# Performance work log

Measured on AMD Instinct MI355X. Metric: run time of the kernel, lower is better.

## Reference

```python
import jax, jax.numpy as jnp
import numpy as np

WS = (2, 7, 7)   # window size (d, h, w)
SS = (1, 3, 3)   # shift size
EPS = 1e-5


def _rel_pos_index(ws):
    d, h, w = np.arange(ws[0]), np.arange(ws[1]), np.arange(ws[2])
    coords = np.stack(np.meshgrid(d, h, w, indexing='ij'))        # (3, wd, wh, ww)
    flat = coords.reshape(3, -1)                                   # (3, N)
    rel = flat[:, :, None] - flat[:, None, :]                      # (3, N, N)
    rel = rel.transpose(1, 2, 0).astype(np.int64)                  # (N, N, 3)
    rel[:, :, 0] += ws[0] - 1
    rel[:, :, 1] += ws[1] - 1
    rel[:, :, 2] += ws[2] - 1
    rel[:, :, 0] *= (2 * ws[1] - 1) * (2 * ws[2] - 1)
    rel[:, :, 1] *= 2 * ws[2] - 1
    return rel.sum(-1)                                             # (N, N)


def _window_partition(x, ws):
    B, D, H, W, C = x.shape
    x = x.reshape(B, D // ws[0], ws[0], H // ws[1], ws[1], W // ws[2], ws[2], C)
    return x.transpose(0, 1, 3, 5, 2, 4, 6, 7).reshape(-1, ws[0] * ws[1] * ws[2], C)


def _window_reverse(win, ws, B, D, H, W):
    x = win.reshape(B, D // ws[0], H // ws[1], W // ws[2], ws[0], ws[1], ws[2], -1)
    return x.transpose(0, 1, 4, 2, 5, 3, 6, 7).reshape(B, D, H, W, -1)


def _attn_mask(D, H, W, ws, ss):
    img = np.zeros((1, D, H, W, 1), np.float32)
    cnt = 0
    for dsl in (slice(None, -ws[0]), slice(-ws[0], -ss[0]), slice(-ss[0], None)):
        for hsl in (slice(None, -ws[1]), slice(-ws[1], -ss[1]), slice(-ss[1], None)):
            for wsl in (slice(None, -ws[2]), slice(-ws[2], -ss[2]), slice(-ss[2], None)):
                img[:, dsl, hsl, wsl, :] = cnt
                cnt += 1
    mw = _window_partition(img, ws)[..., 0]                        # (nW, N)
    am = mw[:, None, :] - mw[:, :, None]                           # (nW, N, N)
    return np.where(am != 0, np.float32(-100.0), np.float32(0.0))


def _ln(x, g, b):
    m = x.mean(-1, keepdims=True)
    v = ((x - m) ** 2).mean(-1, keepdims=True)
    return (x - m) / jnp.sqrt(v + EPS) * g + b


def setup_inputs():
    key = jax.random.key(0)
    B, D, H, W, C = 2, 8, 56, 56, 256
    nH, hidden = 8, 1024
    ks = jax.random.split(key, 8)
    s = 0.02
    inp = {
        'x': jax.random.normal(ks[0], (B, D, H, W, C), jnp.float32),
        'qkv_w': jax.random.normal(ks[1], (3 * C, C), jnp.float32) * s,
        'qkv_b': jnp.zeros((3 * C,), jnp.float32),
        'proj_w': jax.random.normal(ks[2], (C, C), jnp.float32) * s,
        'proj_b': jnp.zeros((C,), jnp.float32),
        'rpb_table': jax.random.normal(ks[3], (3 * 13 * 13, nH), jnp.float32) * s,
        'ln1_g': jnp.ones((C,), jnp.float32),
        'ln1_b': jnp.zeros((C,), jnp.float32),
        'ln2_g': jnp.ones((C,), jnp.float32),
        'ln2_b': jnp.zeros((C,), jnp.float32),
        'fc1_w': jax.random.normal(ks[4], (hidden, C), jnp.float32) * s,
        'fc1_b': jnp.zeros((hidden,), jnp.float32),
        'fc2_w': jax.random.normal(ks[5], (C, hidden), jnp.float32) * s,
        'fc2_b': jnp.zeros((C,), jnp.float32),
        'rel_idx': jnp.asarray(_rel_pos_index(WS), jnp.int32),
        'attn_mask': jnp.asarray(_attn_mask(D, H, W, WS, SS)),
        'num_heads': nH,
    }
    return inp


def reference(x, qkv_w, qkv_b, proj_w, proj_b, rpb_table, ln1_g, ln1_b, ln2_g,
              ln2_b, fc1_w, fc1_b, fc2_w, fc2_b, rel_idx, attn_mask, num_heads):
    B, D, H, W, C = x.shape
    N = WS[0] * WS[1] * WS[2]
    hd = C // num_heads
    scale = hd ** (-0.5)

    shortcut = x
    h = _ln(x, ln1_g, ln1_b)
    # cyclic shift
    h = jnp.roll(h, shift=(-SS[0], -SS[1], -SS[2]), axis=(1, 2, 3))
    win = _window_partition(h, WS)                                 # (B_, N, C)

    qkv = win @ qkv_w.T + qkv_b                                    # (B_, N, 3C)
    qkv = qkv.reshape(-1, N, 3, num_heads, hd).transpose(2, 0, 3, 1, 4)
    q, k, v = qkv[0] * scale, qkv[1], qkv[2]                       # (B_, nH, N, hd)

    attn = jnp.einsum('bhid,bhjd->bhij', q, k)                     # (B_, nH, N, N)
    bias = rpb_table[rel_idx.reshape(-1)].reshape(N, N, num_heads).transpose(2, 0, 1)
    attn = attn + bias[None]
    nW = attn_mask.shape[0]
    attn = attn.reshape(B, nW, num_heads, N, N) + attn_mask[None, :, None]
    attn = jax.nn.softmax(attn.reshape(-1, num_heads, N, N), axis=-1)

    out = jnp.einsum('bhij,bhjd->bhid', attn, v)                   # (B_, nH, N, hd)
    out = out.transpose(0, 2, 1, 3).reshape(-1, N, C)
    out = out @ proj_w.T + proj_b

    xr = _window_reverse(out, WS, B, D, H, W)
    xr = jnp.roll(xr, shift=SS, axis=(1, 2, 3))                    # reverse shift
    x = shortcut + xr

    h2 = _ln(x, ln2_g, ln2_b)
    m = jax.nn.gelu(h2 @ fc1_w.T + fc1_b, approximate=False)
    m = m @ fc2_w.T + fc2_b
    return x + m
```

## Files before the change

kernel.cpp:

```cpp
#include <hip/hip_runtime.h>
#include <hip/hip_bf16.h>
#include <math.h>

#define B_  2
#define D_  8
#define H_  56
#define W_  56
#define C_  256
#define NH_ 8
#define HD_ 32
#define N_  98
#define NWIN_TOT 512
#define TOK (B_*D_*H_*W_)
#define HID 1024

typedef short bf16x8 __attribute__((ext_vector_type(8)));
typedef float f32x4  __attribute__((ext_vector_type(4)));

__device__ __forceinline__ ushort f2b(float f) {
    union { __hip_bfloat16 h; ushort u; } v;
    v.h = __float2bfloat16(f);
    return v.u;
}
__device__ __forceinline__ float b2f(ushort h) {
    union { unsigned u; float f; } v; v.u = ((unsigned)h) << 16;
    return v.f;
}

__device__ __forceinline__ void glds16(const void* gsrc, void* lds_dst) {
    __builtin_amdgcn_global_load_lds(
        (const __attribute__((address_space(1))) unsigned int*)gsrc,
        (__attribute__((address_space(3))) unsigned int*)lds_dst,
        16, 0, 0);
}

__device__ __forceinline__ int tok_of_winrow(int r) {
    int wid  = r / N_;
    int n    = r - wid * N_;
    int b    = wid >> 8;
    int rem  = wid & 255;
    int di   = rem >> 6;
    int hi   = (rem >> 3) & 7;
    int wi   = rem & 7;
    int wd   = n / 49;
    int rem2 = n - wd * 49;
    int wh   = rem2 / 7;
    int ww   = rem2 - wh * 7;
    int d = di * 2 + wd + 1; if (d >= D_) d -= D_;
    int h = hi * 7 + wh + 3; if (h >= H_) h -= H_;
    int w = wi * 7 + ww + 3; if (w >= W_) w -= W_;
    return ((b * D_ + d) * H_ + h) * W_ + w;
}

__device__ __forceinline__ float gelu_fast(float x) {
    float y = 1.5957691216057308f * (x + 0.044715f * x * x * x);
    return x / (1.0f + __expf(-y));
}

template<bool GATHER>
__global__ __launch_bounds__(256)
void ln_kernel(const float* __restrict__ x, const float* __restrict__ g,
               const float* __restrict__ bta, ushort* __restrict__ out, int nrows) {
    int wave = blockIdx.x * 4 + (threadIdx.x >> 6);
    int lane = threadIdx.x & 63;
    if (wave >= nrows) return;
    int srow = GATHER ? tok_of_winrow(wave) : wave;
    float4 v = ((const float4*)(x + (size_t)srow * C_))[lane];
    float s  = v.x + v.y + v.z + v.w;
    float ss = v.x*v.x + v.y*v.y + v.z*v.z + v.w*v.w;
    #pragma unroll
    for (int o = 32; o; o >>= 1) { s += __shfl_xor(s, o); ss += __shfl_xor(ss, o); }
    float mean = s * (1.0f / C_);
    float var  = ss * (1.0f / C_) - mean * mean;
    float rstd = rsqrtf(var + 1e-5f);
    float4 gg = ((const float4*)g)[lane];
    float4 bb = ((const float4*)bta)[lane];
    ushort4 o4;
    o4.x = f2b((v.x - mean) * rstd * gg.x + bb.x);
    o4.y = f2b((v.y - mean) * rstd * gg.y + bb.y);
    o4.z = f2b((v.z - mean) * rstd * gg.z + bb.z);
    o4.w = f2b((v.w - mean) * rstd * gg.w + bb.w);
    ((ushort4*)(out + (size_t)wave * C_))[lane] = o4;
}

#define TB2_WORDS (8 * 8 * 7 * 14 * 64)
__global__ void tbl_kernel(const int* __restrict__ rel_idx,
                           const float* __restrict__ rpb,
                           const float* __restrict__ mask,
                           uint* __restrict__ Tb2) {
    int idx = blockIdx.x * blockDim.x + threadIdx.x;
    if (idx >= TB2_WORDS) return;
    int lane = idx & 63;
    int t    = idx >> 6;
    int nq   = t % 14;  int t2 = t / 14;
    int mi   = t2 % 7;  int ph = t2 / 7;
    int pat  = ph >> 3, hh = ph & 7;
    int nj   = nq >> 1, q = nq & 1;
    int lrow = lane & 15, lgrp = lane >> 4;
    int j  = nj * 16 + lrow;
    int i0 = mi * 16 + lgrp * 4 + q * 2;
    int di = (pat & 1) ? 3 : 0, hi = (pat & 2) ? 7 : 0, wi = (pat & 4) ? 7 : 0;
    int rep = di * 64 + hi * 8 + wi;
    float lo = -1e30f, hv = -1e30f;
    if (j < N_) {
        if (i0 < N_)
            lo = rpb[rel_idx[i0 * N_ + j] * NH_ + hh] + mask[(size_t)rep * (N_*N_) + i0 * N_ + j];
        if (i0 + 1 < N_)
            hv = rpb[rel_idx[(i0+1) * N_ + j] * NH_ + hh] + mask[(size_t)rep * (N_*N_) + (i0+1) * N_ + j];
    }
    Tb2[idx] = (uint)f2b(lo) | ((uint)f2b(hv) << 16);
}

__global__ void f2b4_kernel(const float* __restrict__ s0, ushort* __restrict__ d0, int n0,
                            const float* __restrict__ s1, ushort* __restrict__ d1, int n1,
                            const float* __restrict__ s2, ushort* __restrict__ d2, int n2,
                            const float* __restrict__ s3, ushort* __restrict__ d3, int n3) {
    const float* s; ushort* d; int n;
    switch (blockIdx.y) {
        case 0: s = s0; d = d0; n = n0; break;
        case 1: s = s1; d = d1; n = n1; break;
        case 2: s = s2; d = d2; n = n2; break;
        default: s = s3; d = d3; n = n3; break;
    }
    int i = (blockIdx.x * blockDim.x + threadIdx.x) * 4;
    if (i >= n) return;
    float4 v = *(const float4*)(s + i);
    ushort4 o; o.x = f2b(v.x); o.y = f2b(v.y); o.z = f2b(v.z); o.w = f2b(v.w);
    *(ushort4*)(d + i) = o;
}

template<int MODE>
__global__ __launch_bounds__(256)
void gemm_bf16(const ushort* __restrict__ A, const ushort* __restrict__ Wm,
               const float* __restrict__ bias, void* __restrict__ Cout,
               const void* __restrict__ resid, int M, int K, int Nout) {
    __shared__ __align__(16) char lds[32768];
    char* ldsA = lds;
    char* ldsB = lds + 16384;
    const int tid  = threadIdx.x;
    const int wv   = tid >> 6, lane = tid & 63;
    const int m0   = blockIdx.x * 128, n0 = blockIdx.y * 128;
    const int wrow = (wv >> 1) * 64, wcol = (wv & 1) * 64;
    const int lr8  = lane >> 3, lc = lane & 7;

    f32x4 acc[4][4] = {};

    const ushort* Ag[4]; const ushort* Bg[4];
    #pragma unroll
    for (int i = 0; i < 4; ++i) {
        int row = (wv * 4 + i) * 8 + lr8;
        int gc  = lc ^ (row & 7);
        Ag[i] = A  + (size_t)(m0 + row) * K + gc * 8;
        Bg[i] = Wm + (size_t)(n0 + row) * K + gc * 8;
    }

    for (int k0 = 0; k0 < K; k0 += 64) {
        #pragma unroll
        for (int i = 0; i < 4; ++i) {
            glds16(Ag[i] + k0, ldsA + (wv * 4 + i) * 1024);
            glds16(Bg[i] + k0, ldsB + (wv * 4 + i) * 1024);
        }
        __syncthreads();
        #pragma unroll
        for (int kk = 0; kk < 2; ++kk) {
            bf16x8 af[4], bfr[4];
            #pragma unroll
            for (int i = 0; i < 4; ++i) {
                int r = wrow + i * 16 + (lane & 15);
                int c = (lane >> 4) + kk * 4;
                af[i]  = *(const bf16x8*)(ldsA + r * 128 + ((c ^ (r & 7)) * 16));
                int r2 = wcol + i * 16 + (lane & 15);
                bfr[i] = *(const bf16x8*)(ldsB + r2 * 128 + ((c ^ (r2 & 7)) * 16));
            }
            #pragma unroll
            for (int i = 0; i < 4; ++i)
                #pragma unroll
                for (int j = 0; j < 4; ++j)
                    acc[i][j] = __builtin_amdgcn_mfma_f32_16x16x32_bf16(af[i], bfr[j], acc[i][j], 0, 0, 0);
        }
        __syncthreads();
    }

    int colg[4]; float bv[4];
    #pragma unroll
    for (int j = 0; j < 4; ++j) {
        colg[j] = n0 + wcol + j * 16 + (lane & 15);
        bv[j]   = bias[colg[j]];
    }
    #pragma unroll
    for (int i = 0; i < 4; ++i) {
        #pragma unroll
        for (int r = 0; r < 4; ++r) {
            int rowg = m0 + wrow + i * 16 + ((lane >> 4) << 2) + r;
            #pragma unroll
            for (int j = 0; j < 4; ++j) {
                float v = acc[i][j][r] + bv[j];
                if (MODE == 0) {
                    ((ushort*)Cout)[(size_t)rowg * Nout + colg[j]] = f2b(v);
                } else if (MODE == 2) {
                    ((ushort*)Cout)[(size_t)rowg * Nout + colg[j]] = f2b(gelu_fast(v));
                } else {
                    v += ((const float*)resid)[(size_t)rowg * Nout + colg[j]];
                    ((float*)Cout)[(size_t)rowg * Nout + colg[j]] = v;
                }
            }
        }
    }
}

__global__ __launch_bounds__(256)
void gemm_proj_ln(const ushort* __restrict__ A, const ushort* __restrict__ Wm,
                  const float* __restrict__ pbias, const float* __restrict__ x,
                  const float* __restrict__ g2, const float* __restrict__ b2,
                  float* __restrict__ out, ushort* __restrict__ h2) {
    __shared__ __align__(16) char lds[49152];
    __shared__ float stats[4][64][2];
    char* ldsA = lds;
    char* ldsB = lds + 16384;
    const int tid  = threadIdx.x;
    const int wv   = tid >> 6, lane = tid & 63;
    const int lrow = lane & 15, lgrp = lane >> 4;
    const int m0   = blockIdx.x * 128;
    const int wrow = (wv >> 1) * 64, wcol = (wv & 1) * 128;
    const int lr8  = lane >> 3, lc = lane & 7;

    f32x4 acc[4][8] = {};

    for (int k0 = 0; k0 < 256; k0 += 64) {
        #pragma unroll
        for (int i = 0; i < 4; ++i) {
            int row = (wv * 4 + i) * 8 + lr8;
            int gc  = lc ^ (row & 7);
            glds16(A + (size_t)(m0 + row) * 256 + k0 + gc * 8, ldsA + (wv * 4 + i) * 1024);
        }
        #pragma unroll
        for (int i = 0; i < 8; ++i) {
            int row = (wv * 8 + i) * 8 + lr8;
            int gc  = lc ^ (row & 7);
            glds16(Wm + (size_t)row * 256 + k0 + gc * 8, ldsB + (wv * 8 + i) * 1024);
        }
        __syncthreads();
        #pragma unroll
        for (int kk = 0; kk < 2; ++kk) {
            bf16x8 af[4], bfr[8];
            #pragma unroll
            for (int i = 0; i < 4; ++i) {
                int r = wrow + i * 16 + lrow;
                af[i] = *(const bf16x8*)(ldsA + r * 128 + (((lgrp + kk * 4) ^ (r & 7)) * 16));
            }
            #pragma unroll
            for (int j = 0; j < 8; ++j) {
                int r2 = wcol + j * 16 + lrow;
                bfr[j] = *(const bf16x8*)(ldsB + r2 * 128 + (((lgrp + kk * 4) ^ (r2 & 7)) * 16));
            }
            #pragma unroll
            for (int i = 0; i < 4; ++i)
                #pragma unroll
                for (int j = 0; j < 8; ++j)
                    acc[i][j] = __builtin_amdgcn_mfma_f32_16x16x32_bf16(af[i], bfr[j], acc[i][j], 0, 0, 0);
        }
        __syncthreads();
    }

    int colg[8]; float bvj[8];
    #pragma unroll
    for (int j = 0; j < 8; ++j) {
        colg[j] = wcol + j * 16 + lrow;
        bvj[j]  = pbias[colg[j]];
    }
    int tokr[4][4];

    #pragma unroll
    for (int i = 0; i < 4; ++i) {
        #pragma unroll
        for (int r = 0; r < 4; ++r) {
            int rowg = m0 + wrow + i * 16 + lgrp * 4 + r;
            int tok  = tok_of_winrow(rowg);
            tokr[i][r] = tok;
            float s = 0.f, sq = 0.f;
            #pragma unroll
            for (int j = 0; j < 8; ++j) {
                float v = acc[i][j][r] + bvj[j] + x[(size_t)tok * C_ + colg[j]];
                acc[i][j][r] = v;
                out[(size_t)tok * C_ + colg[j]] = v;
                s += v; sq += v * v;
            }
            #pragma unroll
            for (int o = 1; o < 16; o <<= 1) { s += __shfl_xor(s, o); sq += __shfl_xor(sq, o); }
            if (lrow == 0) {
                int lrw = i * 16 + lgrp * 4 + r;
                stats[wv][lrw][0] = s;
                stats[wv][lrw][1] = sq;
            }
        }
    }
    __syncthreads();

    float gj[8], bj[8];
    #pragma unroll
    for (int j = 0; j < 8; ++j) { gj[j] = g2[colg[j]]; bj[j] = b2[colg[j]]; }
    #pragma unroll
    for (int i = 0; i < 4; ++i) {
        #pragma unroll
        for (int r = 0; r < 4; ++r) {
            int lrw = i * 16 + lgrp * 4 + r;
            float s  = stats[wv][lrw][0] + stats[wv ^ 1][lrw][0];
            float sq = stats[wv][lrw][1] + stats[wv ^ 1][lrw][1];
            float mean = s * (1.0f / 256.0f);
            float var  = sq * (1.0f / 256.0f) - mean * mean;
            float rstd = rsqrtf(var + 1e-5f);
            int tok = tokr[i][r];
            #pragma unroll
            for (int j = 0; j < 8; ++j) {
                float v = (acc[i][j][r] - mean) * rstd * gj[j] + bj[j];
                h2[(size_t)tok * C_ + colg[j]] = f2b(v);
            }
        }
    }
}

#define KOFF 0
#define VOFF 7168
#define POFF 15360
#define SMEM_BYTES 32768
__global__ __launch_bounds__(256)
void attn_mfma(const ushort* __restrict__ qkv, const uint* __restrict__ Tb2,
               ushort* __restrict__ attn_out) {
    __shared__ __align__(16) char smem[SMEM_BYTES];
    ushort (*Pl)[16][136] = (ushort (*)[16][136])(smem + POFF);
    const int b    = blockIdx.x;
    const int wid  = (b & 7) + ((b >> 6) << 3);
    const int hh   = (b >> 3) & 7;
    const int tid  = threadIdx.x;
    const int wv   = tid >> 6, lane = tid & 63;
    const int lrow = lane & 15, lgrp = lane >> 4;
    const float scale = 0.17677669529663687f;

    const ushort* base = qkv + (size_t)wid * N_ * 768 + hh * 32;
    const int rem = wid & 255;
    const int pat = (((rem >> 6) == 3) ? 1 : 0) | ((((rem >> 3) & 7) == 7) ? 2 : 0)
                  | (((rem & 7) == 7) ? 4 : 0);
    const uint* tb2 = Tb2 + (size_t)((pat * 8 + hh) * 7) * 14 * 64 + lane;

    {
        uint4 z = {0, 0, 0, 0};
        uint4* l4 = (uint4*)(smem + 14336);
        for (int i = tid; i < (SMEM_BYTES - 14336) / 16; i += 256) l4[i] = z;
    }
    __syncthreads();

    #pragma unroll
    for (int sect = 0; sect < 2; ++sect) {
        char* dstbase = smem + sect * 7168;
        const ushort* src = base + 256 + sect * 256;
        for (int c = tid; c < 448; c += 256) {
            int r = c >> 2; if (r > 97) r = 97;
            int cc = c & 3;
            glds16(src + (size_t)r * 768 + ((cc ^ (r & 3)) * 8), dstbase + c * 16);
        }
    }
    __syncthreads();

    const int swz = (lgrp ^ (lrow & 3)) << 4;

    bf16x8 kf[7];
    #pragma unroll
    for (int nj = 0; nj < 7; ++nj)
        kf[nj] = *(const bf16x8*)(smem + KOFF + (nj * 16 + lrow) * 64 + swz);

    bf16x8 vf[2][4];
    #pragma unroll
    for (int dt = 0; dt < 2; ++dt)
        #pragma unroll
        for (int kt = 0; kt < 4; ++kt) {
            bf16x8 tmp;
            #pragma unroll
            for (int t = 0; t < 8; ++t) {
                int R = kt * 32 + lgrp * 8 + t;
                int q = dt * 2 + (lrow >> 3);
                tmp[t] = *(const short*)(smem + VOFF + R * 64 +
                                         ((q ^ (t & 3)) << 4) + ((lrow & 7) << 1));
            }
            vf[dt][kt] = tmp;
        }

    for (int mi = wv; mi < 7; mi += 4) {
        const int ibase = mi * 16;

        uint tw[14];
        const uint* tbm = tb2 + mi * 14 * 64;
        #pragma unroll
        for (int u = 0; u < 14; ++u) tw[u] = tbm[u * 64];

        bf16x8 qf = *(const bf16x8*)(base + (size_t)(ibase + lrow) * 768 + lgrp * 8);

        f32x4 s[7];
        #pragma unroll
        for (int nj = 0; nj < 7; ++nj) {
            f32x4 z = {0.f, 0.f, 0.f, 0.f};
            s[nj] = __builtin_amdgcn_mfma_f32_16x16x32_bf16(qf, kf[nj], z, 0, 0, 0);
        }

        #pragma unroll
        for (int nj = 0; nj < 7; ++nj) {
            #pragma unroll
            for (int r = 0; r < 4; ++r) {
                uint w = tw[nj * 2 + (r >> 1)];
                ushort hb = (r & 1) ? (ushort)(w >> 16) : (ushort)(w & 0xffff);
                s[nj][r] = s[nj][r] * scale + b2f(hb);
            }
        }

        float rinv[4];
        #pragma unroll
        for (int r = 0; r < 4; ++r) {
            float acc = 0.f;
            #pragma unroll
            for (int nj = 0; nj < 7; ++nj) {
                float p = __expf(s[nj][r]);
                s[nj][r] = p;
                acc += p;
            }
            #pragma unroll
            for (int o = 1; o < 16; o <<= 1) acc += __shfl_xor(acc, o);
            rinv[r] = 1.f / acc;
        }

        #pragma unroll
        for (int nj = 0; nj < 7; ++nj)
            #pragma unroll
            for (int r = 0; r < 4; ++r)
                Pl[wv][lgrp * 4 + r][nj * 16 + lrow] = f2b(s[nj][r] * rinv[r]);

        f32x4 o0 = {0.f, 0.f, 0.f, 0.f}, o1 = {0.f, 0.f, 0.f, 0.f};
        #pragma unroll
        for (int kt = 0; kt < 4; ++kt) {
            bf16x8 pf = *(const bf16x8*)(&Pl[wv][lrow][kt * 32 + lgrp * 8]);
            o0 = __builtin_amdgcn_mfma_f32_16x16x32_bf16(pf, vf[0][kt], o0, 0, 0, 0);
            o1 = __builtin_amdgcn_mfma_f32_16x16x32_bf16(pf, vf[1][kt], o1, 0, 0, 0);
        }

        #pragma unroll
        for (int r = 0; r < 4; ++r) {
            int i = ibase + lgrp * 4 + r;
            if (i < N_) {
                size_t rb = ((size_t)(wid * N_ + i)) * C_ + hh * 32;
                attn_out[rb + lrow]      = f2b(o0[r]);
                attn_out[rb + 16 + lrow] = f2b(o1[r]);
            }
        }
    }
}

extern "C" void kernel_launch(void* const* d_in, const int* in_sizes, int n_in,
                              void* d_out, int out_size, void* d_ws, size_t ws_size,
                              hipStream_t stream) {
    const float* x      = (const float*)d_in[0];
    const float* qkv_w  = (const float*)d_in[1];
    const float* qkv_b  = (const float*)d_in[2];
    const float* proj_w = (const float*)d_in[3];
    const float* proj_b = (const float*)d_in[4];
    const float* rpb    = (const float*)d_in[5];
    const float* ln1_g  = (const float*)d_in[6];
    const float* ln1_b  = (const float*)d_in[7];
    const float* ln2_g  = (const float*)d_in[8];
    const float* ln2_b  = (const float*)d_in[9];
    const float* fc1_w  = (const float*)d_in[10];
    const float* fc1_b  = (const float*)d_in[11];
    const float* fc2_w  = (const float*)d_in[12];
    const float* fc2_b  = (const float*)d_in[13];
    const int*   rel_idx= (const int*)d_in[14];
    const float* mask   = (const float*)d_in[15];
    float* out = (float*)d_out;

    char* ws = (char*)d_ws;
    ushort* regionA = (ushort*)ws;
    ushort* regionB = (ushort*)(ws + (size_t)TOK * HID * 2);
    ushort* wq  = (ushort*)(ws + (size_t)TOK * HID * 2 + (size_t)TOK * C_ * 2);
    ushort* wp  = wq + 768 * 256;
    ushort* w1  = wp + 256 * 256;
    ushort* w2  = w1 + HID * 256;
    uint*   Tb2 = (uint*)(w2 + 256 * HID);
    ushort* h2buf = (ushort*)((char*)Tb2 + TB2_WORDS * 4);

    tbl_kernel<<<(TB2_WORDS + 255) / 256, 256, 0, stream>>>(rel_idx, rpb, mask, Tb2);
    {
        dim3 g(256, 4);
        f2b4_kernel<<<g, 256, 0, stream>>>(qkv_w, wq, 768 * 256,
                                           proj_w, wp, 256 * 256,
                                           fc1_w, w1, HID * 256,
                                           fc2_w, w2, 256 * HID);
    }

    ln_kernel<true><<<TOK / 4, 256, 0, stream>>>(x, ln1_g, ln1_b, regionB, TOK);

    {
        dim3 g(TOK / 128, 768 / 128);
        gemm_bf16<0><<<g, 256, 0, stream>>>(regionB, wq, qkv_b, regionA, nullptr, TOK, 256, 768);
    }

    attn_mfma<<<NWIN_TOT * NH_, 256, 0, stream>>>(regionA, Tb2, regionB);

    gemm_proj_ln<<<TOK / 128, 256, 0, stream>>>(regionB, wp, proj_b, x,
                                                ln2_g, ln2_b, out, h2buf);

    {
        dim3 g(TOK / 128, HID / 128);
        gemm_bf16<2><<<g, 256, 0, stream>>>(h2buf, w1, fc1_b, regionA, nullptr, TOK, 256, HID);
    }

    {
        dim3 g(TOK / 128, 256 / 128);
        gemm_bf16<3><<<g, 256, 0, stream>>>(regionA, w2, fc2_b, out, out, TOK, HID, 256);
    }
}
```

Baseline: 266.2 us.

## Fuse MLP fc1+GELU+fc2 into one kernel and stage QKV stores through LDS

Replaces the two MLP GEMM launches with one fused kernel. Each 64-token block keeps its LN2 output in LDS, computes fc1 in 128-wide hidden chunks, applies GELU into LDS, and accumulates fc2 in registers, so the 1024-wide hidden activation never goes to global memory. The fused kernel reads w1 and w2 fragments straight from global memory, without LDS staging or double buffering, which may make it latency-bound. Separately, the QKV GEMM epilogue now writes results through a swizzled LDS tile so that global stores are 16-byte coalesced.

New measurement: 342.8 us. +28.8%, slower.

```diff
diff --git a/kernel.cpp b/kernel.cpp
--- a/kernel.cpp
+++ b/kernel.cpp
@@ -129,11 +129,10 @@
     *(ushort4*)(d + i) = o;
 }
 
-template<int MODE>
 __global__ __launch_bounds__(256)
-void gemm_bf16(const ushort* __restrict__ A, const ushort* __restrict__ Wm,
-               const float* __restrict__ bias, void* __restrict__ Cout,
-               const void* __restrict__ resid, int M, int K, int Nout) {
+void gemm_qkv(const ushort* __restrict__ A, const ushort* __restrict__ Wm,
+              const float* __restrict__ bias, ushort* __restrict__ Cout,
+              int K, int Nout) {
     __shared__ __align__(16) char lds[32768];
     char* ldsA = lds;
     char* ldsB = lds + 16384;
@@ -142,6 +141,7 @@
     const int m0   = blockIdx.x * 128, n0 = blockIdx.y * 128;
     const int wrow = (wv >> 1) * 64, wcol = (wv & 1) * 64;
     const int lr8  = lane >> 3, lc = lane & 7;
+    const int lrow = lane & 15, lgrp = lane >> 4;
 
     f32x4 acc[4][4] = {};
 
@@ -166,10 +166,10 @@
             bf16x8 af[4], bfr[4];
             #pragma unroll
             for (int i = 0; i < 4; ++i) {
-                int r = wrow + i * 16 + (lane & 15);
-                int c = (lane >> 4) + kk * 4;
+                int r = wrow + i * 16 + lrow;
+                int c = lgrp + kk * 4;
                 af[i]  = *(const bf16x8*)(ldsA + r * 128 + ((c ^ (r & 7)) * 16));
-                int r2 = wcol + i * 16 + (lane & 15);
+                int r2 = wcol + i * 16 + lrow;
                 bfr[i] = *(const bf16x8*)(ldsB + r2 * 128 + ((c ^ (r2 & 7)) * 16));
             }
             #pragma unroll
@@ -181,30 +181,32 @@
         __syncthreads();
     }
 
-    int colg[4]; float bv[4];
-    #pragma unroll
-    for (int j = 0; j < 4; ++j) {
-        colg[j] = n0 + wcol + j * 16 + (lane & 15);
-        bv[j]   = bias[colg[j]];
-    }
+    float bv[4];
+    #pragma unroll
+    for (int j = 0; j < 4; ++j) bv[j] = bias[n0 + wcol + j * 16 + lrow];
+
     #pragma unroll
     for (int i = 0; i < 4; ++i) {
         #pragma unroll
         for (int r = 0; r < 4; ++r) {
-            int rowg = m0 + wrow + i * 16 + ((lane >> 4) << 2) + r;
+            int row_l = wrow + i * 16 + lgrp * 4 + r;
             #pragma unroll
             for (int j = 0; j < 4; ++j) {
-                float v = acc[i][j][r] + bv[j];
-                if (MODE == 0) {
-                    ((ushort*)Cout)[(size_t)rowg * Nout + colg[j]] = f2b(v);
-                } else if (MODE == 2) {
-                    ((ushort*)Cout)[(size_t)rowg * Nout + colg[j]] = f2b(gelu_fast(v));
-                } else {
-                    v += ((const float*)resid)[(size_t)rowg * Nout + colg[j]];
-                    ((float*)Cout)[(size_t)rowg * Nout + colg[j]] = v;
-                }
-            }
-        }
+                int col_l = wcol + j * 16 + lrow;
+                int cchunk = (col_l >> 3) ^ (row_l & 7);
+                *(ushort*)(lds + row_l * 256 + (cchunk << 4) + ((col_l & 7) << 1)) =
+                    f2b(acc[i][j][r] + bv[j]);
+            }
+        }
+    }
+    __syncthreads();
+
+    #pragma unroll
+    for (int it = 0; it < 8; ++it) {
+        int li  = tid + it * 256;
+        int row = li >> 4, c = li & 15;
+        uint4 v = *(const uint4*)(lds + row * 256 + ((c ^ (row & 7)) << 4));
+        *(uint4*)(Cout + (size_t)(m0 + row) * Nout + n0 + c * 8) = v;
     }
 }
 
@@ -314,6 +316,114 @@
             for (int j = 0; j < 8; ++j) {
                 float v = (acc[i][j][r] - mean) * rstd * gj[j] + bj[j];
                 h2[(size_t)tok * C_ + colg[j]] = f2b(v);
+            }
+        }
+    }
+}
+
+__global__ __launch_bounds__(256)
+void gemm_mlp(const ushort* __restrict__ h2, const ushort* __restrict__ w1,
+              const float* __restrict__ b1, const ushort* __restrict__ w2,
+              const float* __restrict__ b2, float* __restrict__ out) {
+    __shared__ __align__(16) char ldsA[32768];
+    __shared__ __align__(16) char ldsH[16384];
+    const int tid  = threadIdx.x;
+    const int wv   = tid >> 6, lane = tid & 63;
+    const int lrow = lane & 15, lgrp = lane >> 4;
+    const int m0   = blockIdx.x * 64;
+    const int wr   = wv >> 1, wc = wv & 1;
+
+    #pragma unroll
+    for (int it = 0; it < 8; ++it) {
+        int ci  = tid + it * 256;
+        int row = ci >> 5, d = ci & 31;
+        glds16(h2 + (size_t)(m0 + row) * 256 + ((d ^ (row & 7)) * 8), ldsA + ci * 16);
+    }
+    __syncthreads();
+
+    f32x4 acc2[4][4] = {};
+
+    for (int hc = 0; hc < 8; ++hc) {
+        f32x4 acc1[2][4] = {};
+        #pragma unroll
+        for (int ks = 0; ks < 8; ++ks) {
+            bf16x8 af[2], bfr[4];
+            #pragma unroll
+            for (int i = 0; i < 2; ++i) {
+                int row = wr * 32 + i * 16 + lrow;
+                int c   = ks * 4 + lgrp;
+                af[i] = *(const bf16x8*)(ldsA + row * 512 + ((c ^ (row & 7)) << 4));
+            }
+            #pragma unroll
+            for (int j = 0; j < 4; ++j) {
+                int hr = hc * 128 + wc * 64 + j * 16 + lrow;
+                bfr[j] = *(const bf16x8*)(w1 + (size_t)hr * 256 + ks * 32 + lgrp * 8);
+            }
+            #pragma unroll
+            for (int i = 0; i < 2; ++i)
+                #pragma unroll
+                for (int j = 0; j < 4; ++j)
+                    acc1[i][j] = __builtin_amdgcn_mfma_f32_16x16x32_bf16(af[i], bfr[j], acc1[i][j], 0, 0, 0);
+        }
+
+        float b1v[4];
+        #pragma unroll
+        for (int j = 0; j < 4; ++j) b1v[j] = b1[hc * 128 + wc * 64 + j * 16 + lrow];
+
+        __syncthreads();
+        #pragma unroll
+        for (int i = 0; i < 2; ++i) {
+            #pragma unroll
+            for (int j = 0; j < 4; ++j) {
+                int hid_l = wc * 64 + j * 16 + lrow;
+                #pragma unroll
+                for (int r = 0; r < 4; ++r) {
+                    int hrow = wr * 32 + i * 16 + lgrp * 4 + r;
+                    float v = gelu_fast(acc1[i][j][r] + b1v[j]);
+                    int cchunk = (hid_l >> 3) ^ (hrow & 7);
+                    *(ushort*)(ldsH + hrow * 256 + (cchunk << 4) + ((hid_l & 7) << 1)) = f2b(v);
+                }
+            }
+        }
+        __syncthreads();
+
+        #pragma unroll
+        for (int ks = 0; ks < 4; ++ks) {
+            bf16x8 af2[4], bf2[4];
+            #pragma unroll
+            for (int i = 0; i < 4; ++i) {
+                int row = i * 16 + lrow;
+                int c   = ks * 4 + lgrp;
+                af2[i] = *(const bf16x8*)(ldsH + row * 256 + ((c ^ (row & 7)) << 4));
+            }
+            #pragma unroll
+            for (int j = 0; j < 4; ++j) {
+                int cr = wv * 64 + j * 16 + lrow;
+                bf2[j] = *(const bf16x8*)(w2 + (size_t)cr * 1024 + hc * 128 + ks * 32 + lgrp * 8);
+            }
+            #pragma unroll
+            for (int i = 0; i < 4; ++i)
+                #pragma unroll
+                for (int j = 0; j < 4; ++j)
+                    acc2[i][j] = __builtin_amdgcn_mfma_f32_16x16x32_bf16(af2[i], bf2[j], acc2[i][j], 0, 0, 0);
+        }
+    }
+
+    float b2v[4]; int cg[4];
+    #pragma unroll
+    for (int j = 0; j < 4; ++j) {
+        cg[j]  = wv * 64 + j * 16 + lrow;
+        b2v[j] = b2[cg[j]];
+    }
+    #pragma unroll
+    for (int i = 0; i < 4; ++i) {
+        #pragma unroll
+        for (int r = 0; r < 4; ++r) {
+            int row = m0 + i * 16 + lgrp * 4 + r;
+            #pragma unroll
+            for (int j = 0; j < 4; ++j) {
+                float v = acc2[i][j][r] + b2v[j] + out[(size_t)row * C_ + cg[j]];
+                out[(size_t)row * C_ + cg[j]] = v;
             }
         }
     }
@@ -496,7 +606,7 @@
 
     {
         dim3 g(TOK / 128, 768 / 128);
-        gemm_bf16<0><<<g, 256, 0, stream>>>(regionB, wq, qkv_b, regionA, nullptr, TOK, 256, 768);
+        gemm_qkv<<<g, 256, 0, stream>>>(regionB, wq, qkv_b, regionA, 256, 768);
     }
 
     attn_mfma<<<NWIN_TOT * NH_, 256, 0, stream>>>(regionA, Tb2, regionB);
@@ -504,13 +614,5 @@
     gemm_proj_ln<<<TOK / 128, 256, 0, stream>>>(regionB, wp, proj_b, x,
                                                 ln2_g, ln2_b, out, h2buf);
 
-    {
-        dim3 g(TOK / 128, HID / 128);
-        gemm_bf16<2><<<g, 256, 0, stream>>>(h2buf, w1, fc1_b, regionA, nullptr, TOK, 256, HID);
-    }
-
-    {
-        dim3 g(TOK / 128, 256 / 128);
-        gemm_bf16<3><<<g, 256, 0, stream>>>(regionA, w2, fc2_b, out, out, TOK, HID, 256);
-    }
-}
+    gemm_mlp<<<TOK / 64, 256, 0, stream>>>(h2buf, w1, fc1_b, w2, fc2_b, out);
+}
```

## Double-buffer GEMM LDS tiles, linearize grid for M-tile locality, inline bf16 rounding

Applied to the files above, without the earlier changes.

The generic bf16 GEMM now double-buffers its A/B tiles in 64KB of LDS, issuing global-to-LDS loads for the next k-step before computing on the current one. This drops one barrier per iteration and overlaps load latency with MFMA work. The grid is flattened to 1D with the N-tile index varying fastest, so blocks sharing an A row-tile run close together and reuse it in cache. The float-to-bf16 conversion is replaced by a manual round-to-nearest-even bit trick, which skips NaN handling. Doubling LDS per block may lower occupancy.

After: 263.8 us. No clear change (-0.9%).

```diff
diff --git a/kernel.cpp b/kernel.cpp
--- a/kernel.cpp
+++ b/kernel.cpp
@@ -18,9 +18,9 @@
 typedef float f32x4  __attribute__((ext_vector_type(4)));
 
 __device__ __forceinline__ ushort f2b(float f) {
-    union { __hip_bfloat16 h; ushort u; } v;
-    v.h = __float2bfloat16(f);
-    return v.u;
+    union { float f; unsigned u; } v; v.f = f;
+    unsigned r = v.u + 0x7fff + ((v.u >> 16) & 1);
+    return (ushort)(r >> 16);
 }
 __device__ __forceinline__ float b2f(ushort h) {
     union { unsigned u; float f; } v; v.u = ((unsigned)h) << 16;
@@ -134,42 +134,58 @@
 void gemm_bf16(const ushort* __restrict__ A, const ushort* __restrict__ Wm,
                const float* __restrict__ bias, void* __restrict__ Cout,
                const void* __restrict__ resid, int M, int K, int Nout) {
-    __shared__ __align__(16) char lds[32768];
-    char* ldsA = lds;
-    char* ldsB = lds + 16384;
+    __shared__ __align__(16) char lds[65536];
     const int tid  = threadIdx.x;
     const int wv   = tid >> 6, lane = tid & 63;
-    const int m0   = blockIdx.x * 128, n0 = blockIdx.y * 128;
+    const int nby  = Nout >> 7;
+    const int bx   = blockIdx.x / nby, by = blockIdx.x - bx * nby;
+    const int m0   = bx * 128, n0 = by * 128;
     const int wrow = (wv >> 1) * 64, wcol = (wv & 1) * 64;
     const int lr8  = lane >> 3, lc = lane & 7;
+    const int lrow = lane & 15, lgrp = lane >> 4;
 
     f32x4 acc[4][4] = {};
 
     const ushort* Ag[4]; const ushort* Bg[4];
+    int ldoff[4];
     #pragma unroll
     for (int i = 0; i < 4; ++i) {
         int row = (wv * 4 + i) * 8 + lr8;
         int gc  = lc ^ (row & 7);
         Ag[i] = A  + (size_t)(m0 + row) * K + gc * 8;
         Bg[i] = Wm + (size_t)(n0 + row) * K + gc * 8;
-    }
-
-    for (int k0 = 0; k0 < K; k0 += 64) {
-        #pragma unroll
-        for (int i = 0; i < 4; ++i) {
-            glds16(Ag[i] + k0, ldsA + (wv * 4 + i) * 1024);
-            glds16(Bg[i] + k0, ldsB + (wv * 4 + i) * 1024);
-        }
-        __syncthreads();
+        ldoff[i] = (wv * 4 + i) * 1024;
+    }
+
+    const int nk = K >> 6;
+    #pragma unroll
+    for (int i = 0; i < 4; ++i) {
+        glds16(Ag[i], lds + ldoff[i]);
+        glds16(Bg[i], lds + 16384 + ldoff[i]);
+    }
+    __syncthreads();
+
+    int cur = 0;
+    for (int t = 0; t < nk; ++t) {
+        if (t + 1 < nk) {
+            char* nb = lds + (cur ^ 1) * 32768;
+            #pragma unroll
+            for (int i = 0; i < 4; ++i) {
+                glds16(Ag[i] + (t + 1) * 64, nb + ldoff[i]);
+                glds16(Bg[i] + (t + 1) * 64, nb + 16384 + ldoff[i]);
+            }
+        }
+        char* ldsA = lds + cur * 32768;
+        char* ldsB = ldsA + 16384;
         #pragma unroll
         for (int kk = 0; kk < 2; ++kk) {
             bf16x8 af[4], bfr[4];
             #pragma unroll
             for (int i = 0; i < 4; ++i) {
-                int r = wrow + i * 16 + (lane & 15);
-                int c = (lane >> 4) + kk * 4;
+                int r = wrow + i * 16 + lrow;
+                int c = lgrp + kk * 4;
                 af[i]  = *(const bf16x8*)(ldsA + r * 128 + ((c ^ (r & 7)) * 16));
-                int r2 = wcol + i * 16 + (lane & 15);
+                int r2 = wcol + i * 16 + lrow;
                 bfr[i] = *(const bf16x8*)(ldsB + r2 * 128 + ((c ^ (r2 & 7)) * 16));
             }
             #pragma unroll
@@ -179,19 +195,20 @@
                     acc[i][j] = __builtin_amdgcn_mfma_f32_16x16x32_bf16(af[i], bfr[j], acc[i][j], 0, 0, 0);
         }
         __syncthreads();
+        cur ^= 1;
     }
 
     int colg[4]; float bv[4];
     #pragma unroll
     for (int j = 0; j < 4; ++j) {
-        colg[j] = n0 + wcol + j * 16 + (lane & 15);
+        colg[j] = n0 + wcol + j * 16 + lrow;
         bv[j]   = bias[colg[j]];
     }
     #pragma unroll
     for (int i = 0; i < 4; ++i) {
         #pragma unroll
         for (int r = 0; r < 4; ++r) {
-            int rowg = m0 + wrow + i * 16 + ((lane >> 4) << 2) + r;
+            int rowg = m0 + wrow + i * 16 + (lgrp << 2) + r;
             #pragma unroll
             for (int j = 0; j < 4; ++j) {
                 float v = acc[i][j][r] + bv[j];
@@ -494,23 +511,17 @@
 
     ln_kernel<true><<<TOK / 4, 256, 0, stream>>>(x, ln1_g, ln1_b, regionB, TOK);
 
-    {
-        dim3 g(TOK / 128, 768 / 128);
-        gemm_bf16<0><<<g, 256, 0, stream>>>(regionB, wq, qkv_b, regionA, nullptr, TOK, 256, 768);
-    }
+    gemm_bf16<0><<<(TOK / 128) * 6, 256, 0, stream>>>(regionB, wq, qkv_b, regionA,
+                                                      nullptr, TOK, 256, 768);
 
     attn_mfma<<<NWIN_TOT * NH_, 256, 0, stream>>>(regionA, Tb2, regionB);
 
     gemm_proj_ln<<<TOK / 128, 256, 0, stream>>>(regionB, wp, proj_b, x,
                                                 ln2_g, ln2_b, out, h2buf);
 
-    {
-        dim3 g(TOK / 128, HID / 128);
-        gemm_bf16<2><<<g, 256, 0, stream>>>(h2buf, w1, fc1_b, regionA, nullptr, TOK, 256, HID);
-    }
-
-    {
-        dim3 g(TOK / 128, 256 / 128);
-        gemm_bf16<3><<<g, 256, 0, stream>>>(regionA, w2, fc2_b, out, out, TOK, HID, 256);
-    }
-}
+    gemm_bf16<2><<<(TOK / 128) * 8, 256, 0, stream>>>(h2buf, w1, fc1_b, regionA,
+                                                      nullptr, TOK, 256, HID);
+
+    gemm_bf16<3><<<(TOK / 128) * 2, 256, 0, stream>>>(regionA, w2, fc2_b, out,
+                                                      out, TOK, HID, 256);
+}
```

## Transpose MFMA output to vectorize GEMM epilogues and swap grid order

Applied to the files above, without the earlier changes.

Swaps the MFMA operand order so each lane holds four consecutive output columns of one row. This lets the GEMM and proj+LN epilogues use float4 and packed-bf16 stores and loads instead of scattered scalar accesses. It also adds a hardware packed bf16 conversion instruction and reorders the grid so blocks sharing an A row-tile run together, which should improve cache reuse of activations. It changes the LN reduction layout, which adds risk of correctness errors in the stats exchange.

Result: slower. 291.5 us (+9.5%).

```diff
diff --git a/kernel.cpp b/kernel.cpp
--- a/kernel.cpp
+++ b/kernel.cpp
@@ -18,13 +18,18 @@
 typedef float f32x4  __attribute__((ext_vector_type(4)));
 
 __device__ __forceinline__ ushort f2b(float f) {
-    union { __hip_bfloat16 h; ushort u; } v;
-    v.h = __float2bfloat16(f);
-    return v.u;
+    union { float f; unsigned u; } v; v.f = f;
+    unsigned r = v.u + 0x7fff + ((v.u >> 16) & 1);
+    return (ushort)(r >> 16);
 }
 __device__ __forceinline__ float b2f(ushort h) {
     union { unsigned u; float f; } v; v.u = ((unsigned)h) << 16;
     return v.f;
+}
+__device__ __forceinline__ uint pk2(float a, float b) {
+    uint r;
+    asm("v_cvt_pk_bf16_f32 %0, %1, %2" : "=v"(r) : "v"(a), "v"(b));
+    return r;
 }
 
 __device__ __forceinline__ void glds16(const void* gsrc, void* lds_dst) {
@@ -75,12 +80,10 @@
     float rstd = rsqrtf(var + 1e-5f);
     float4 gg = ((const float4*)g)[lane];
     float4 bb = ((const float4*)bta)[lane];
-    ushort4 o4;
-    o4.x = f2b((v.x - mean) * rstd * gg.x + bb.x);
-    o4.y = f2b((v.y - mean) * rstd * gg.y + bb.y);
-    o4.z = f2b((v.z - mean) * rstd * gg.z + bb.z);
-    o4.w = f2b((v.w - mean) * rstd * gg.w + bb.w);
-    ((ushort4*)(out + (size_t)wave * C_))[lane] = o4;
+    uint2 o2;
+    o2.x = pk2((v.x - mean) * rstd * gg.x + bb.x, (v.y - mean) * rstd * gg.y + bb.y);
+    o2.y = pk2((v.z - mean) * rstd * gg.z + bb.z, (v.w - mean) * rstd * gg.w + bb.w);
+    ((uint2*)(out + (size_t)wave * C_))[lane] = o2;
 }
 
 #define TB2_WORDS (8 * 8 * 7 * 14 * 64)
@@ -125,8 +128,8 @@
     int i = (blockIdx.x * blockDim.x + threadIdx.x) * 4;
     if (i >= n) return;
     float4 v = *(const float4*)(s + i);
-    ushort4 o; o.x = f2b(v.x); o.y = f2b(v.y); o.z = f2b(v.z); o.w = f2b(v.w);
-    *(ushort4*)(d + i) = o;
+    uint2 o; o.x = pk2(v.x, v.y); o.y = pk2(v.z, v.w);
+    *(uint2*)(d + i) = o;
 }
 
 template<int MODE>
@@ -139,9 +142,10 @@
     char* ldsB = lds + 16384;
     const int tid  = threadIdx.x;
     const int wv   = tid >> 6, lane = tid & 63;
-    const int m0   = blockIdx.x * 128, n0 = blockIdx.y * 128;
+    const int n0   = blockIdx.x * 128, m0 = blockIdx.y * 128;
     const int wrow = (wv >> 1) * 64, wcol = (wv & 1) * 64;
     const int lr8  = lane >> 3, lc = lane & 7;
+    const int lrow = lane & 15, lgrp = lane >> 4;
 
     f32x4 acc[4][4] = {};
 
@@ -166,43 +170,47 @@
             bf16x8 af[4], bfr[4];
             #pragma unroll
             for (int i = 0; i < 4; ++i) {
-                int r = wrow + i * 16 + (lane & 15);
-                int c = (lane >> 4) + kk * 4;
+                int r = wrow + i * 16 + lrow;
+                int c = lgrp + kk * 4;
                 af[i]  = *(const bf16x8*)(ldsA + r * 128 + ((c ^ (r & 7)) * 16));
-                int r2 = wcol + i * 16 + (lane & 15);
+                int r2 = wcol + i * 16 + lrow;
                 bfr[i] = *(const bf16x8*)(ldsB + r2 * 128 + ((c ^ (r2 & 7)) * 16));
             }
             #pragma unroll
             for (int i = 0; i < 4; ++i)
                 #pragma unroll
                 for (int j = 0; j < 4; ++j)
-                    acc[i][j] = __builtin_amdgcn_mfma_f32_16x16x32_bf16(af[i], bfr[j], acc[i][j], 0, 0, 0);
+                    acc[i][j] = __builtin_amdgcn_mfma_f32_16x16x32_bf16(bfr[j], af[i], acc[i][j], 0, 0, 0);
         }
         __syncthreads();
     }
 
-    int colg[4]; float bv[4];
-    #pragma unroll
-    for (int j = 0; j < 4; ++j) {
-        colg[j] = n0 + wcol + j * 16 + (lane & 15);
-        bv[j]   = bias[colg[j]];
-    }
+    float4 bv4[4];
+    #pragma unroll
+    for (int j = 0; j < 4; ++j)
+        bv4[j] = *(const float4*)(bias + n0 + wcol + j * 16 + lgrp * 4);
     #pragma unroll
     for (int i = 0; i < 4; ++i) {
-        #pragma unroll
-        for (int r = 0; r < 4; ++r) {
-            int rowg = m0 + wrow + i * 16 + ((lane >> 4) << 2) + r;
-            #pragma unroll
-            for (int j = 0; j < 4; ++j) {
-                float v = acc[i][j][r] + bv[j];
-                if (MODE == 0) {
-                    ((ushort*)Cout)[(size_t)rowg * Nout + colg[j]] = f2b(v);
-                } else if (MODE == 2) {
-                    ((ushort*)Cout)[(size_t)rowg * Nout + colg[j]] = f2b(gelu_fast(v));
-                } else {
-                    v += ((const float*)resid)[(size_t)rowg * Nout + colg[j]];
-                    ((float*)Cout)[(size_t)rowg * Nout + colg[j]] = v;
-                }
+        size_t rowoff = (size_t)(m0 + wrow + i * 16 + lrow) * Nout;
+        #pragma unroll
+        for (int j = 0; j < 4; ++j) {
+            int cbase = n0 + wcol + j * 16 + lgrp * 4;
+            float v0 = acc[i][j][0] + bv4[j].x;
+            float v1 = acc[i][j][1] + bv4[j].y;
+            float v2 = acc[i][j][2] + bv4[j].z;
+            float v3 = acc[i][j][3] + bv4[j].w;
+            if (MODE == 2) {
+                v0 = gelu_fast(v0); v1 = gelu_fast(v1);
+                v2 = gelu_fast(v2); v3 = gelu_fast(v3);
+            }
+            if (MODE == 0 || MODE == 2) {
+                uint2 pv; pv.x = pk2(v0, v1); pv.y = pk2(v2, v3);
+                *(uint2*)((ushort*)Cout + rowoff + cbase) = pv;
+            } else {
+                float4 rv = *(const float4*)((const float*)resid + rowoff + cbase);
+                float4 ov; ov.x = v0 + rv.x; ov.y = v1 + rv.y;
+                ov.z = v2 + rv.z; ov.w = v3 + rv.w;
+                *(float4*)((float*)Cout + rowoff + cbase) = ov;
             }
         }
     }
@@ -257,64 +265,71 @@
             for (int i = 0; i < 4; ++i)
                 #pragma unroll
                 for (int j = 0; j < 8; ++j)
-                    acc[i][j] = __builtin_amdgcn_mfma_f32_16x16x32_bf16(af[i], bfr[j], acc[i][j], 0, 0, 0);
+                    acc[i][j] = __builtin_amdgcn_mfma_f32_16x16x32_bf16(bfr[j], af[i], acc[i][j], 0, 0, 0);
         }
         __syncthreads();
     }
 
-    int colg[8]; float bvj[8];
+    int colb[8]; float4 pb4[8];
     #pragma unroll
     for (int j = 0; j < 8; ++j) {
-        colg[j] = wcol + j * 16 + lrow;
-        bvj[j]  = pbias[colg[j]];
-    }
-    int tokr[4][4];
+        colb[j] = wcol + j * 16 + lgrp * 4;
+        pb4[j]  = *(const float4*)(pbias + colb[j]);
+    }
+    int tokr[4]; float rs[4], rsq[4];
 
     #pragma unroll
     for (int i = 0; i < 4; ++i) {
-        #pragma unroll
-        for (int r = 0; r < 4; ++r) {
-            int rowg = m0 + wrow + i * 16 + lgrp * 4 + r;
-            int tok  = tok_of_winrow(rowg);
-            tokr[i][r] = tok;
-            float s = 0.f, sq = 0.f;
-            #pragma unroll
-            for (int j = 0; j < 8; ++j) {
-                float v = acc[i][j][r] + bvj[j] + x[(size_t)tok * C_ + colg[j]];
-                acc[i][j][r] = v;
-                out[(size_t)tok * C_ + colg[j]] = v;
-                s += v; sq += v * v;
-            }
-            #pragma unroll
-            for (int o = 1; o < 16; o <<= 1) { s += __shfl_xor(s, o); sq += __shfl_xor(sq, o); }
-            if (lrow == 0) {
-                int lrw = i * 16 + lgrp * 4 + r;
-                stats[wv][lrw][0] = s;
-                stats[wv][lrw][1] = sq;
-            }
+        int rowg = m0 + wrow + i * 16 + lrow;
+        int tok  = tok_of_winrow(rowg);
+        tokr[i] = tok;
+        float s = 0.f, sq = 0.f;
+        #pragma unroll
+        for (int j = 0; j < 8; ++j) {
+            float4 xr = *(const float4*)(x + (size_t)tok * C_ + colb[j]);
+            float4 v;
+            v.x = acc[i][j][0] + pb4[j].x + xr.x;
+            v.y = acc[i][j][1] + pb4[j].y + xr.y;
+            v.z = acc[i][j][2] + pb4[j].z + xr.z;
+            v.w = acc[i][j][3] + pb4[j].w + xr.w;
+            acc[i][j][0] = v.x; acc[i][j][1] = v.y;
+            acc[i][j][2] = v.z; acc[i][j][3] = v.w;
+            *(float4*)(out + (size_t)tok * C_ + colb[j]) = v;
+            s  += v.x + v.y + v.z + v.w;
+            sq += v.x*v.x + v.y*v.y + v.z*v.z + v.w*v.w;
+        }
+        s  += __shfl_xor(s, 16);  s  += __shfl_xor(s, 32);
+        sq += __shfl_xor(sq, 16); sq += __shfl_xor(sq, 32);
+        rs[i] = s; rsq[i] = sq;
+        if (lgrp == 0) {
+            stats[wv][i * 16 + lrow][0] = s;
+            stats[wv][i * 16 + lrow][1] = sq;
         }
     }
     __syncthreads();
 
-    float gj[8], bj[8];
-    #pragma unroll
-    for (int j = 0; j < 8; ++j) { gj[j] = g2[colg[j]]; bj[j] = b2[colg[j]]; }
+    float4 g4[8], bb4[8];
+    #pragma unroll
+    for (int j = 0; j < 8; ++j) {
+        g4[j]  = *(const float4*)(g2 + colb[j]);
+        bb4[j] = *(const float4*)(b2 + colb[j]);
+    }
     #pragma unroll
     for (int i = 0; i < 4; ++i) {
-        #pragma unroll
-        for (int r = 0; r < 4; ++r) {
-            int lrw = i * 16 + lgrp * 4 + r;
-            float s  = stats[wv][lrw][0] + stats[wv ^ 1][lrw][0];
-            float sq = stats[wv][lrw][1] + stats[wv ^ 1][lrw][1];
-            float mean = s * (1.0f / 256.0f);
-            float var  = sq * (1.0f / 256.0f) - mean * mean;
-            float rstd = rsqrtf(var + 1e-5f);
-            int tok = tokr[i][r];
-            #pragma unroll
-            for (int j = 0; j < 8; ++j) {
-                float v = (acc[i][j][r] - mean) * rstd * gj[j] + bj[j];
-                h2[(size_t)tok * C_ + colg[j]] = f2b(v);
-            }
+        float s  = rs[i]  + stats[wv ^ 1][i * 16 + lrow][0];
+        float sq = rsq[i] + stats[wv ^ 1][i * 16 + lrow][1];
+        float mean = s * (1.0f / 256.0f);
+        float var  = sq * (1.0f / 256.0f) - mean * mean;
+        float rstd = rsqrtf(var + 1e-5f);
+        int tok = tokr[i];
+        #pragma unroll
+        for (int j = 0; j < 8; ++j) {
+            float v0 = (acc[i][j][0] - mean) * rstd * g4[j].x + bb4[j].x;
+            float v1 = (acc[i][j][1] - mean) * rstd * g4[j].y + bb4[j].y;
+            float v2 = (acc[i][j][2] - mean) * rstd * g4[j].z + bb4[j].z;
+            float v3 = (acc[i][j][3] - mean) * rstd * g4[j].w + bb4[j].w;
+            uint2 pv; pv.x = pk2(v0, v1); pv.y = pk2(v2, v3);
+            *(uint2*)(h2 + (size_t)tok * C_ + colb[j]) = pv;
         }
     }
 }
@@ -495,8 +510,9 @@
     ln_kernel<true><<<TOK / 4, 256, 0, stream>>>(x, ln1_g, ln1_b, regionB, TOK);
 
     {
-        dim3 g(TOK / 128, 768 / 128);
-        gemm_bf16<0><<<g, 256, 0, stream>>>(regionB, wq, qkv_b, regionA, nullptr, TOK, 256, 768);
+        dim3 g(768 / 128, TOK / 128);
+        gemm_bf16<0><<<g, 256, 0, stream>>>(regionB, wq, qkv_b, regionA,
+                                            nullptr, TOK, 256, 768);
     }
 
     attn_mfma<<<NWIN_TOT * NH_, 256, 0, stream>>>(regionA, Tb2, regionB);
@@ -505,12 +521,14 @@
                                                 ln2_g, ln2_b, out, h2buf);
 
     {
-        dim3 g(TOK / 128, HID / 128);
-        gemm_bf16<2><<<g, 256, 0, stream>>>(h2buf, w1, fc1_b, regionA, nullptr, TOK, 256, HID);
+        dim3 g(HID / 128, TOK / 128);
+        gemm_bf16<2><<<g, 256, 0, stream>>>(h2buf, w1, fc1_b, regionA,
+                                            nullptr, TOK, 256, HID);
     }
 
     {
-        dim3 g(TOK / 128, 256 / 128);
-        gemm_bf16<3><<<g, 256, 0, stream>>>(regionA, w2, fc2_b, out, out, TOK, HID, 256);
-    }
-}
+        dim3 g(256 / 128, TOK / 128);
+        gemm_bf16<3><<<g, 256, 0, stream>>>(regionA, w2, fc2_b, out,
+                                            out, TOK, HID, 256);
+    }
+}
```
